# Performance work log

Measured on AMD Instinct MI355X. Metric: run time of the kernel, lower is better.

The kernel has to match this reference:

```python
import jax, jax.numpy as jnp
import numpy as np

# config
BSZ, L_, DM = 4, 2048, 1024
H, G, P, N, R = 16, 4, 64, 64, 2
RATIO = H // G            # 4
E, K = 64, 2              # kmoe experts / top_k
DPROJ = H * P * 2 + G * N * R * 2 + G * 3  # 3084


def rms(x, w, eps=1e-5):
    return x * jax.lax.rsqrt(jnp.mean(x * x, axis=-1, keepdims=True) + eps) * w


def kron_moe(x, router_w, A_e, B_e, scale, bias, d1, d2, o1, o2, k):
    # x: [..., d1*d2] -> [..., o1*o2]
    orig = x.shape
    xf = x.reshape(-1, d1 * d2)
    logits = xf @ router_w.T                       # [T, E]
    vals, idx = jax.lax.top_k(logits, k)           # [T, k]
    probs = jax.nn.softmax(vals, axis=-1)
    xs = xf.reshape(-1, d1, d2)
    # Y[t,k,o,p] = sum_ij A[t,k,o,i] x[t,i,j] B[t,k,p,j]
    Y = jnp.einsum('tkoi,tij,tkpj->tkop', A_e[idx], xs, B_e[idx])
    out = jnp.sum(Y * probs[:, :, None, None], axis=1).reshape(orig[:-1] + (o1 * o2,))
    return out * scale + bias


def setup_inputs() -> dict:
    key = jax.random.key(0)
    ks = jax.random.split(key, 12)
    r = lambda k, s, sc: jax.random.normal(k, s, jnp.float32) * sc
    return dict(
        u=jax.random.normal(ks[0], (BSZ, L_, DM), jnp.float32),
        in_proj_w=r(ks[1], (DPROJ, DM), 0.02),
        in_proj_b=jnp.zeros((DPROJ,), jnp.float32),
        xup_router=r(ks[2], (E, P), 0.02),
        xup_A=r(ks[3], (E, 8, 8), 0.1),
        xup_B=r(ks[4], (E, 16, 8), 0.1),
        xup_scale=jnp.ones((1,), jnp.float32),
        xup_bias=jnp.zeros((P * R,), jnp.float32),
        ydown_w=r(ks[5], (P, P * R), 0.02),
        oup_router=r(ks[6], (E, H * P), 0.02),
        oup_A=r(ks[7], (E, 32, 32), 0.05),
        oup_B=r(ks[8], (E, 32, 32), 0.05),
        oup_scale=jnp.ones((1,), jnp.float32),
        oup_bias=jnp.zeros((DM,), jnp.float32),
        theta_log=r(ks[9], (G, N // 2), 1.0),
        D=jnp.ones((H,), jnp.float32),
        normB_w=jnp.ones((N * R,), jnp.float32),
        normC_w=jnp.ones((N * R,), jnp.float32),
        bias_B=jnp.zeros((G, N, R), jnp.float32),
        bias_C=jnp.zeros((G, N, R), jnp.float32),
        pregate_w=jnp.ones((H * P,), jnp.float32),
    )


def reference(u, in_proj_w, in_proj_b, xup_router, xup_A, xup_B, xup_scale, xup_bias,
              ydown_w, oup_router, oup_A, oup_B, oup_scale, oup_bias,
              theta_log, D, normB_w, normC_w, bias_B, bias_C, pregate_w):
    B, L, _ = u.shape
    HP, GNR = H * P, G * N * R
    proj = u @ in_proj_w.T + in_proj_b
    splits = np.cumsum([HP, HP, GNR, GNR, G, G])
    z, x_p, Bp, Cp, dt, A_p, lam = jnp.split(proj, splits, axis=-1)
    dt = jax.nn.softplus(dt)                       # [B,L,G]
    A = -jnp.exp(A_p)                              # [B,L,G]
    theta = jnp.exp(theta_log)                     # [G,N/2]
    Bp = rms(Bp.reshape(B, L, G, N * R), normB_w).reshape(B, L, G, N, R) + bias_B
    Cp = rms(Cp.reshape(B, L, G, N * R), normC_w).reshape(B, L, G, N, R) + bias_C
    angles_g = jnp.cumsum(dt[..., None] * theta[None, None], axis=1)   # [B,L,G,N/2]
    rep = lambda v: jnp.repeat(v, RATIO, axis=2)   # group -> head broadcast
    angles = rep(angles_g)                         # [B,L,H,N/2]
    dt_h = rep(dt[..., None])                      # [B,L,H,1]
    A_h = rep(A[..., None])                        # [B,L,H,1]
    B_h, C_h = rep(Bp), rep(Cp)                    # [B,L,H,N,R]
    cos = jnp.cos(angles)[..., None]
    sin = jnp.sin(angles)[..., None]

    def rotate(v):
        re, im = v[..., 0::2, :], v[..., 1::2, :]
        return jnp.stack([re * cos - im * sin, re * sin + im * cos], axis=-2).reshape(v.shape)

    B_rot, C_rot = rotate(B_h), rotate(C_h)
    x = kron_moe(x_p.reshape(B, L, H, P), xup_router, xup_A, xup_B, xup_scale, xup_bias,
                 8, 8, 8, 16, K).reshape(B, L, H, P, R)
    alpha = jnp.exp(dt_h * A_h)[..., None]         # [B,L,H,1,1]

    mv = lambda v: jnp.moveaxis(v, 1, 0)           # time-major for scan

    def step(h, xs):
        Br, Cr, xt, at, dtt = xs
        in_sig = jnp.einsum('bhnr,bhpr->bhnp', Br, xt)
        h = h * at + dtt[..., None] * in_sig
        y_t = jnp.einsum('bhnp,bhnr->bhpr', h, Cr)
        return h, y_t

    h0 = jnp.zeros((B, H, N, P), u.dtype)
    _, ys = jax.lax.scan(step, h0, (mv(B_rot), mv(C_rot), mv(x), mv(alpha), mv(dt_h)))
    y = jnp.moveaxis(ys, 0, 1)                     # [B,L,H,P,R]
    y = (y.reshape(B, L, H, P * R) @ ydown_w.T).reshape(B, L, H * P)
    y = rms(y + x_p * jnp.repeat(D, P), pregate_w) * jax.nn.sigmoid(z)
    out = kron_moe(y, oup_router, oup_A, oup_B, oup_scale, oup_bias, 32, 32, 32, 32, K)
    return out
```

## Files before the change

kernel.cpp:

```cpp
#include <hip/hip_runtime.h>
#include <hip/hip_bf16.h>
#include <math.h>

namespace {
constexpr int kB = 4, kL = 2048, kDM = 1024;
constexpr int kH = 16, kG = 4;
constexpr int kDPROJ = 3084;
constexpr int COL_Z = 0, COL_XP = 1024, COL_B = 2048, COL_C = 2560, COL_DT = 3072, COL_A = 3076;
constexpr int kTOK = kB * kL;
constexpr int kNC = kL / 64;
constexpr int kNPAD = 3200;
constexpr float kLOG2E = 1.4426950408889634f;
}

typedef __attribute__((ext_vector_type(8))) __bf16 bf16x8;
typedef __attribute__((ext_vector_type(8))) unsigned short u16x8;
typedef __attribute__((ext_vector_type(4))) float f32x4;

#define GLDS16(gp, lp)                                                          \
  __builtin_amdgcn_global_load_lds(                                             \
      (const __attribute__((address_space(1))) void*)(gp),                      \
      (__attribute__((address_space(3))) void*)(lp), 16, 0, 0)

__device__ __forceinline__ unsigned short bf16_rne(float f) {
  unsigned u = __builtin_bit_cast(unsigned, f);
  unsigned r = u + 0x7fffu + ((u >> 16) & 1u);
  return (unsigned short)(r >> 16);
}
__device__ __forceinline__ void split2(float f, unsigned short& h, unsigned short& l) {
  unsigned short hh = bf16_rne(f);
  float hf = __builtin_bit_cast(float, (unsigned)hh << 16);
  h = hh;
  l = bf16_rne(f - hf);
}
__device__ __forceinline__ bf16x8 ldsb8(const unsigned short* p) {
  return __builtin_bit_cast(bf16x8, *(const u16x8*)p);
}

__global__ __launch_bounds__(256) void k_split_u(const float* __restrict__ X,
                                                 unsigned short* __restrict__ hi,
                                                 unsigned short* __restrict__ lo) {
  int i = blockIdx.x * 256 + threadIdx.x;
  float4 x = ((const float4*)X)[i];
  float xs[4] = {x.x, x.y, x.z, x.w};
  ushort4 hv, lv;
  unsigned short hq[4], lq[4];
#pragma unroll
  for (int q = 0; q < 4; ++q) split2(xs[q], hq[q], lq[q]);
  hv.x = hq[0]; hv.y = hq[1]; hv.z = hq[2]; hv.w = hq[3];
  lv.x = lq[0]; lv.y = lq[1]; lv.z = lq[2]; lv.w = lq[3];
  ((ushort4*)hi)[i] = hv;
  ((ushort4*)lo)[i] = lv;
}

__global__ __launch_bounds__(256) void k_split_w(const float* __restrict__ X,
                                                 unsigned short* __restrict__ hi,
                                                 unsigned short* __restrict__ lo) {
  int i = blockIdx.x * 256 + threadIdx.x;
  int row = i >> 8;
  float4 x = make_float4(0.f, 0.f, 0.f, 0.f);
  if (row < kDPROJ) x = ((const float4*)X)[i];
  float xs[4] = {x.x, x.y, x.z, x.w};
  ushort4 hv, lv;
  unsigned short hq[4], lq[4];
#pragma unroll
  for (int q = 0; q < 4; ++q) split2(xs[q], hq[q], lq[q]);
  hv.x = hq[0]; hv.y = hq[1]; hv.z = hq[2]; hv.w = hq[3];
  lv.x = lq[0]; lv.y = lq[1]; lv.z = lq[2]; lv.w = lq[3];
  ((ushort4*)hi)[i] = hv;
  ((ushort4*)lo)[i] = lv;
}

__global__ __launch_bounds__(256) void k_inproj_mfma(
    const unsigned short* __restrict__ Uhi, const unsigned short* __restrict__ Ulo,
    const unsigned short* __restrict__ Whi, const unsigned short* __restrict__ Wlo,
    const float* __restrict__ bias, float* __restrict__ proj,
    float* __restrict__ dtA) {
  __shared__ unsigned short lds_u[16384];
  const int tid = threadIdx.x;
  const int wave = tid >> 6, lane = tid & 63;
  const int wm = wave >> 1, wn = wave & 1;
  const int row0 = blockIdx.x * 128, col0 = blockIdx.y * 128;
  const int fr = lane & 15, kq = lane >> 4;

  f32x4 acc[4][4];
#pragma unroll
  for (int i = 0; i < 4; ++i)
#pragma unroll
    for (int j = 0; j < 4; ++j) acc[i][j] = (f32x4){0.f, 0.f, 0.f, 0.f};

  const int s0 = wave * 64 + lane;

  for (int k0 = 0; k0 < kDM; k0 += 32) {
#pragma unroll
    for (int q = 0; q < 2; ++q) {
      const int slot = q * 256 + s0;
      const int r = slot >> 2;
      const int ce = ((slot & 3) ^ ((r >> 1) & 3)) * 8;
      const size_t ao = (size_t)(row0 + r) * kDM + k0 + ce;
      const size_t bo = (size_t)(col0 + r) * kDM + k0 + ce;
      const int lb = (q * 256 + wave * 64) * 16;
      GLDS16(Uhi + ao, (char*)lds_u + lb);
      GLDS16(Ulo + ao, (char*)lds_u + 8192 + lb);
      GLDS16(Whi + bo, (char*)lds_u + 16384 + lb);
      GLDS16(Wlo + bo, (char*)lds_u + 24576 + lb);
    }
    __syncthreads();
    bf16x8 ahi[4], alo[4], bhi[4], blo[4];
#pragma unroll
    for (int mi = 0; mi < 4; ++mi) {
      int r = wm * 64 + mi * 16 + fr;
      int off = r * 32 + ((kq ^ ((r >> 1) & 3)) * 8);
      ahi[mi] = ldsb8(lds_u + off);
      alo[mi] = ldsb8(lds_u + 4096 + off);
    }
#pragma unroll
    for (int ni = 0; ni < 4; ++ni) {
      int r = wn * 64 + ni * 16 + fr;
      int off = r * 32 + ((kq ^ ((r >> 1) & 3)) * 8);
      bhi[ni] = ldsb8(lds_u + 8192 + off);
      blo[ni] = ldsb8(lds_u + 12288 + off);
    }
#pragma unroll
    for (int mi = 0; mi < 4; ++mi)
#pragma unroll
      for (int ni = 0; ni < 4; ++ni) {
        acc[mi][ni] = __builtin_amdgcn_mfma_f32_16x16x32_bf16(ahi[mi], bhi[ni], acc[mi][ni], 0, 0, 0);
        acc[mi][ni] = __builtin_amdgcn_mfma_f32_16x16x32_bf16(ahi[mi], blo[ni], acc[mi][ni], 0, 0, 0);
        acc[mi][ni] = __builtin_amdgcn_mfma_f32_16x16x32_bf16(alo[mi], bhi[ni], acc[mi][ni], 0, 0, 0);
      }
    __syncthreads();
  }

  const int orow = row0 + wm * 64, ocol = col0 + wn * 64;
#pragma unroll
  for (int mi = 0; mi < 4; ++mi)
#pragma unroll
    for (int ni = 0; ni < 4; ++ni) {
      int cg = ocol + ni * 16 + fr;
      if (cg < kDPROJ) {
        float bv = bias[cg];
#pragma unroll
        for (int r = 0; r < 4; ++r) {
          int rg = orow + mi * 16 + kq * 4 + r;
          float v = acc[mi][ni][r] + bv;
          proj[(size_t)rg * kDPROJ + cg] = v;
          if (cg >= COL_DT && cg < COL_DT + 8)
            dtA[(size_t)rg * 8 + (cg - COL_DT)] = v;
        }
      }
    }
}

__global__ __launch_bounds__(256) void k_dtprep(const float* __restrict__ dtA,
                                                float* __restrict__ dtg,
                                                float* __restrict__ cumalog,
                                                double* __restrict__ cumdt) {
  int bg = blockIdx.x;
  int b = bg / kG, g = bg % kG;
  int tid = threadIdx.x;
  __shared__ double s_dt[256], s_al[256];
  double loc_dt[8], loc_al[8];
  double sdt = 0.0, sal = 0.0;
#pragma unroll
  for (int q = 0; q < 8; ++q) {
    int t = tid * 8 + q;
    size_t i = (size_t)(b * kL + t) * 8;
    float rd = dtA[i + g];
    float ra = dtA[i + 4 + g];
    float dt = rd > 20.f ? rd : log1pf(expf(rd));
    float al = -expf(ra) * dt;
    dtg[(size_t)(b * kL + t) * kG + g] = dt;
    sdt += (double)dt; loc_dt[q] = sdt;
    sal += (double)al; loc_al[q] = sal;
  }
  s_dt[tid] = sdt; s_al[tid] = sal;
  __syncthreads();
  for (int off = 1; off < 256; off <<= 1) {
    double a = 0.0, c = 0.0;
    if (tid >= off) { a = s_dt[tid - off]; c = s_al[tid - off]; }
    __syncthreads();
    s_dt[tid] += a; s_al[tid] += c;
    __syncthreads();
  }
  double base_dt = tid ? s_dt[tid - 1] : 0.0;
  double base_al = tid ? s_al[tid - 1] : 0.0;
#pragma unroll
  for (int q = 0; q < 8; ++q) {
    int t = tid * 8 + q;
    size_t idx = (size_t)(b * kL + t) * kG + g;
    cumdt[idx] = base_dt + loc_dt[q];
    cumalog[idx] = (float)(base_al + loc_al[q]);
  }
}

__global__ __launch_bounds__(256) void k_angles(const double* __restrict__ cumdt,
                                                const float* __restrict__ theta_log,
                                                float* __restrict__ cs_tab) {
  int idx = blockIdx.x * 256 + threadIdx.x;
  int tok = idx >> 7, gk = idx & 127, g = gk >> 5, k = gk & 31;
  double theta = exp((double)theta_log[g * 32 + k]);
  double ang = theta * cumdt[(size_t)tok * kG + g];
  const double twopi = 6.283185307179586476925286766559;
  double rem = ang - floor(ang / twopi) * twopi;
  cs_tab[(size_t)idx * 2] = cosf((float)rem);
  cs_tab[(size_t)idx * 2 + 1] = sinf((float)rem);
}

__global__ __launch_bounds__(1024) void k_rotate(float* __restrict__ proj,
                                                 const float* __restrict__ cs_tab,
                                                 const float* __restrict__ normB_w,
                                                 const float* __restrict__ normC_w,
                                                 const float* __restrict__ bias_B,
                                                 const float* __restrict__ bias_C) {
  int tok = blockIdx.x;
  int tid = threadIdx.x;
  __shared__ float buf[1024];
  __shared__ float red[16];
  size_t rowoff = (size_t)tok * kDPROJ;
  int g = tid >> 8;
  int half = (tid >> 7) & 1;
  int j = tid & 127;
  int wave = tid >> 6;
  int col = (half ? COL_C : COL_B) + g * 128 + j;
  float v = proj[rowoff + col];
  float ss = v * v;
  for (int o = 1; o < 64; o <<= 1) ss += __shfl_xor(ss, o);
  if ((tid & 63) == 0) red[wave] = ss;
  __syncthreads();
  float tot = red[wave] + red[wave ^ 1];
  float scale = rsqrtf(tot / 128.f + 1e-5f);
  const float* nw = half ? normC_w : normB_w;
  const float* bb = half ? bias_C : bias_B;
  float nv = v * scale * nw[j] + bb[g * 128 + j];
  buf[tid] = nv;
  __syncthreads();
  float other = buf[tid ^ 2];
  int n = j >> 1;
  int k = n >> 1;
  bool isRe = (n & 1) == 0;
  const float* cs = cs_tab + (((size_t)tok * kG + g) * 32 + k) * 2;
  float cc = cs[0], sn = cs[1];
  float out = isRe ? (nv * cc - other * sn) : (other * sn + nv * cc);
  proj[rowoff + col] = out;
}

__global__ __launch_bounds__(256) void k_xup(const float* __restrict__ proj,
                                             const float* __restrict__ router,
                                             const float* __restrict__ Ae,
                                             const float* __restrict__ Be,
                                             const float* __restrict__ scale_,
                                             const float* __restrict__ bias_,
                                             float* __restrict__ xmoe) {
  int wave = threadIdx.x >> 6, lane = threadIdx.x & 63;
  int unit = blockIdx.x * 4 + wave;
  int tok = unit >> 4, h = unit & 15;
  __shared__ double Rd[64][65];
  __shared__ double xs_d[4][64];
  __shared__ float  xs_f[4][65];
  for (int m = threadIdx.x; m < 4096; m += 256)
    Rd[m >> 6][m & 63] = (double)router[m];
  float xv = proj[(size_t)tok * kDPROJ + COL_XP + h * 64 + lane];
  xs_d[wave][lane] = (double)xv;
  xs_f[wave][lane] = xv;
  __syncthreads();
  double a0 = 0.0, a1 = 0.0, a2 = 0.0, a3 = 0.0;
#pragma unroll
  for (int d = 0; d < 64; d += 4) {
    a0 += Rd[lane][d + 0] * xs_d[wave][d + 0];
    a1 += Rd[lane][d + 1] * xs_d[wave][d + 1];
    a2 += Rd[lane][d + 2] * xs_d[wave][d + 2];
    a3 += Rd[lane][d + 3] * xs_d[wave][d + 3];
  }
  float logit = (float)((a0 + a1) + (a2 + a3));
  float v1 = logit; int i1 = lane;
  for (int o = 1; o < 64; o <<= 1) {
    float vv = __shfl_xor(v1, o); int ii = __shfl_xor(i1, o);
    if (vv > v1 || (vv == v1 && ii < i1)) { v1 = vv; i1 = ii; }
  }
  float lm = (lane == i1) ? -INFINITY : logit;
  float v2 = lm; int i2 = lane;
  for (int o = 1; o < 64; o <<= 1) {
    float vv = __shfl_xor(v2, o); int ii = __shfl_xor(i2, o);
    if (vv > v2 || (vv == v2 && ii < i2)) { v2 = vv; i2 = ii; }
  }
  int e1 = __builtin_amdgcn_readfirstlane(i1);
  int e2 = __builtin_amdgcn_readfirstlane(i2);
  float e12 = expf(v2 - v1);
  float p1 = 1.f / (1.f + e12), p2 = e12 / (1.f + e12);
  const int p = lane & 15, o = lane >> 4;
  float out0 = 0.f, out1 = 0.f;
#pragma unroll
  for (int kk = 0; kk < 2; ++kk) {
    int e = kk ? e2 : e1;
    float pw = kk ? p2 : p1;
    const float4* Bp = (const float4*)(Be + (size_t)e * 128 + p * 8);
    float4 b0 = Bp[0], b1 = Bp[1];
    const float4* Ar = (const float4*)(Ae + (size_t)e * 64);
    float4 A0a = Ar[o * 2], A0b = Ar[o * 2 + 1];
    float4 A1a = Ar[(o + 4) * 2], A1b = Ar[(o + 4) * 2 + 1];
    float Ar0[8] = {A0a.x, A0a.y, A0a.z, A0a.w, A0b.x, A0b.y, A0b.z, A0b.w};
    float Ar1[8] = {A1a.x, A1a.y, A1a.z, A1a.w, A1b.x, A1b.y, A1b.z, A1b.w};
    float y0 = 0.f, y1 = 0.f;
#pragma unroll
    for (int i = 0; i < 8; ++i) {
      const float* xp = &xs_f[wave][i * 8];
      float t = xp[0] * b0.x + xp[1] * b0.y + xp[2] * b0.z + xp[3] * b0.w
              + xp[4] * b1.x + xp[5] * b1.y + xp[6] * b1.z + xp[7] * b1.w;
      y0 += Ar0[i] * t;
      y1 += Ar1[i] * t;
    }
    out0 += pw * y0;
    out1 += pw * y1;
  }
  float sc = scale_[0];
  size_t ob = (size_t)unit * 128;
  xmoe[ob + lane] = out0 * sc + bias_[lane];
  xmoe[ob + lane + 64] = out1 * sc + bias_[lane + 64];
}

namespace { constexpr int SK = 136; }
__global__ __launch_bounds__(256) void k_passA(const float* __restrict__ proj,
                                               const float* __restrict__ xmoe,
                                               const float* __restrict__ dtg,
                                               const float* __restrict__ cumalog,
                                               float* __restrict__ hstate) {
  __shared__ unsigned short sBh[64 * SK];
  __shared__ unsigned short sBl[64 * SK];
  __shared__ unsigned short sXh[64 * SK];
  __shared__ unsigned short sXl[64 * SK];
  __shared__ float wv[64];
  int bid = blockIdx.x;
  int c = bid & 31, h = (bid >> 5) & 15, b = bid >> 9, g = h >> 2;
  int tid = threadIdx.x;
  const int wave = tid >> 6, lane = tid & 63;
  const int fr = lane & 15, kq = lane >> 4;
  int base = c * 64;
  size_t tok0 = (size_t)b * kL + base;
  if (tid < 64) {
    float ca_last = cumalog[(tok0 + 63) * kG + g];
    float ca_s = cumalog[(tok0 + tid) * kG + g];
    float dt = dtg[(tok0 + tid) * kG + g];
    wv[tid] = expf(ca_last - ca_s) * dt;
  }
  __syncthreads();
  for (int m = tid; m < 8192; m += 256) {
    int s = m >> 7, j = m & 127;
    int k = s * 2 + (j & 1), n = j >> 1;
    unsigned short hh, ll;
    float bval = proj[(tok0 + s) * kDPROJ + COL_B + g * 128 + j] * wv[s];
    split2(bval, hh, ll);
    sBh[n * SK + k] = hh; sBl[n * SK + k] = ll;
    float xval = xmoe[((tok0 + s) * kH + h) * (size_t)128 + j];
    split2(xval, hh, ll);
    sXh[n * SK + k] = hh; sXl[n * SK + k] = ll;
  }
  __syncthreads();
  const int n0 = wave * 16;
  f32x4 acc[4];
#pragma unroll
  for (int j = 0; j < 4; ++j) acc[j] = (f32x4){0.f, 0.f, 0.f, 0.f};
#pragma unroll
  for (int ks = 0; ks < 4; ++ks) {
    int kb = ks * 32 + kq * 8;
    int offA = (n0 + fr) * SK + kb;
    bf16x8 ah = ldsb8(sBh + offA);
    bf16x8 al = ldsb8(sBl + offA);
#pragma unroll
    for (int ni = 0; ni < 4; ++ni) {
      int offB = (ni * 16 + fr) * SK + kb;
      bf16x8 bh = ldsb8(sXh + offB);
      bf16x8 bl = ldsb8(sXl + offB);
      acc[ni] = __builtin_amdgcn_mfma_f32_16x16x32_bf16(ah, bh, acc[ni], 0, 0, 0);
      acc[ni] = __builtin_amdgcn_mfma_f32_16x16x32_bf16(ah, bl, acc[ni], 0, 0, 0);
      acc[ni] = __builtin_amdgcn_mfma_f32_16x16x32_bf16(al, bh, acc[ni], 0, 0, 0);
    }
  }
  float* out = hstate + (size_t)bid * 4096;
#pragma unroll
  for (int ni = 0; ni < 4; ++ni)
#pragma unroll
    for (int r = 0; r < 4; ++r) {
      int n = n0 + kq * 4 + r;
      int p = ni * 16 + fr;
      out[n * 64 + p] = acc[ni][r];
    }
}

__global__ __launch_bounds__(256) void k_passB(float* __restrict__ hstate,
                                               const float* __restrict__ cumalog) {
  int bid = blockIdx.x;
  int q8 = bid & 7, bh = bid >> 3;
  int b = bh >> 4, g = (bh & 15) >> 2;
  int tid = threadIdx.x;
  float hrun[2] = {0.f, 0.f};
  float* Hbase = hstate + (size_t)bh * 32 * 4096 + q8 * 512;
  for (int c = 0; c < 32; ++c) {
    float ca_last = cumalog[((size_t)b * kL + c * 64 + 63) * kG + g];
    float ca_prev = c ? cumalog[((size_t)b * kL + c * 64 - 1) * kG + g] : 0.f;
    float Dc = expf(ca_last - ca_prev);
    float* Hc = Hbase + (size_t)c * 4096;
#pragma unroll
    for (int q = 0; q < 2; ++q) {
      int idx = tid + q * 256;
      float local = Hc[idx];
      Hc[idx] = hrun[q];
      hrun[q] = Dc * hrun[q] + local;
    }
  }
}

namespace {
constexpr int SC = 72;
constexpr int SG = 136;
constexpr int SH = 72;
constexpr int SW = 66;
}
__global__ __launch_bounds__(1024) void k_passC(const float* __restrict__ proj,
                                                const float* __restrict__ xmoe,
                                                const float* __restrict__ dtg,
                                                const float* __restrict__ cumalog,
                                                const float* __restrict__ hstate,
                                                const float* __restrict__ ydown,
                                                float* __restrict__ outY) {
  __shared__ __align__(16) char smem[162560];
  unsigned short* sCh = (unsigned short*)smem;
  unsigned short* sCl = sCh + 128 * SC;
  unsigned short* sBh = (unsigned short*)(smem + 36864);
  unsigned short* sBl = sBh + 128 * SC;
  float*          sW  = (float*)(smem + 73728);
  unsigned short* sHh = (unsigned short*)(smem + 73728);
  unsigned short* sHl = sHh + 64 * SH;
  unsigned short* sGh = (unsigned short*)(smem + 92160);
  unsigned short* sGl = sGh + 128 * SG;
  float* sca  = (float*)(smem + 161792);
  float* sdts = sca + 64;
  float* selx = sdts + 64;
  unsigned short* sXh  = (unsigned short*)smem;
  unsigned short* sXl  = sXh + 64 * SG;
  unsigned short* sWdh = (unsigned short*)(smem + 36864);
  unsigned short* sWdl = sWdh + 64 * SG;
  unsigned short* sYh  = (unsigned short*)(smem + 92160);
  unsigned short* sYl  = sYh + 64 * SG;

  int bid = blockIdx.x;
  int c = bid & 31, h = (bid >> 5) & 15, b = bid >> 9, g = h >> 2;
  int tid = threadIdx.x;
  const int wave = tid >> 6, lane = tid & 63;
  const int fr = lane & 15, kq = lane >> 4;
  int base = c * 64;
  size_t tok0 = (size_t)b * kL + base;
  size_t projBase = tok0 * kDPROJ;

  if (tid < 64) {
    float ca_prev = base ? cumalog[(tok0 - 1) * kG + g] : 0.f;
    float ca_t = cumalog[(tok0 + tid) * kG + g];
    sca[tid] = ca_t;
    sdts[tid] = dtg[(tok0 + tid) * kG + g];
    selx[tid] = exp2f((ca_t - ca_prev) * kLOG2E);
  }
  for (int m = tid; m < 8192; m += 1024) {
    int s = m >> 7, j = m & 127;
    int row = s * 2 + (j & 1), col = j >> 1;
    unsigned short hh, ll;
    float cv = proj[projBase + (size_t)s * kDPROJ + COL_C + g * 128 + j];
    split2(cv, hh, ll);
    sCh[row * SC + col] = hh; sCl[row * SC + col] = ll;
    float bv = proj[projBase + (size_t)s * kDPROJ + COL_B + g * 128 + j];
    split2(bv, hh, ll);
    sBh[row * SC + col] = hh; sBl[row * SC + col] = ll;
  }
  __syncthreads();

  for (int m = tid; m < 4096; m += 1024) {
    int t = m >> 6, s = m & 63;
    float w = (s <= t) ? sdts[s] * exp2f((sca[t] - sca[s]) * kLOG2E) : 0.f;
    sW[t * SW + s] = w;
  }
  const int rowA0 = (wave & 7) * 16;
  const int colH = wave >> 3;
  f32x4 gacc[4];
#pragma unroll
  for (int j = 0; j < 4; ++j) gacc[j] = (f32x4){0.f, 0.f, 0.f, 0.f};
#pragma unroll
  for (int ks = 0; ks < 2; ++ks) {
    int kb = ks * 32 + kq * 8;
    int offA = (rowA0 + fr) * SC + kb;
    bf16x8 ah = ldsb8(sCh + offA);
    bf16x8 al = ldsb8(sCl + offA);
#pragma unroll
    for (int ni = 0; ni < 4; ++ni) {
      int off = (colH * 64 + ni * 16 + fr) * SC + kb;
      bf16x8 bh = ldsb8(sBh + off);
      bf16x8 bl = ldsb8(sBl + off);
      gacc[ni] = __builtin_amdgcn_mfma_f32_16x16x32_bf16(ah, bh, gacc[ni], 0, 0, 0);
      gacc[ni] = __builtin_amdgcn_mfma_f32_16x16x32_bf16(ah, bl, gacc[ni], 0, 0, 0);
      gacc[ni] = __builtin_amdgcn_mfma_f32_16x16x32_bf16(al, bh, gacc[ni], 0, 0, 0);
    }
  }
  __syncthreads();

#pragma unroll
  for (int ni = 0; ni < 4; ++ni) {
    int colg = colH * 64 + ni * 16 + fr;
    int s = colg >> 1;
#pragma unroll
    for (int r = 0; r < 4; ++r) {
      int rowg = rowA0 + kq * 4 + r;
      int t = rowg >> 1;
      float gm = gacc[ni][r] * sW[t * SW + s];
      unsigned short hh, ll;
      split2(gm, hh, ll);
      sGh[rowg * SG + colg] = hh;
      sGl[rowg * SG + colg] = ll;
    }
  }
  __syncthreads();

  for (int m = tid; m < 4096; m += 1024) {
    int n = m >> 6, p = m & 63;
    float v = hstate[(size_t)bid * 4096 + m];
    unsigned short hh, ll;
    split2(v, hh, ll);
    sHh[p * SH + n] = hh;
    sHl[p * SH + n] = ll;
  }
  __syncthreads();

  f32x4 yac[2];
#pragma unroll
  for (int j = 0; j < 2; ++j) yac[j] = (f32x4){0.f, 0.f, 0.f, 0.f};
#pragma unroll
  for (int ks = 0; ks < 2; ++ks) {
    int kb = ks * 32 + kq * 8;
    int offA = (rowA0 + fr) * SC + kb;
    bf16x8 ah = ldsb8(sCh + offA);
    bf16x8 al = ldsb8(sCl + offA);
#pragma unroll
    for (int ni = 0; ni < 2; ++ni) {
      int off = (colH * 32 + ni * 16 + fr) * SH + kb;
      bf16x8 bh = ldsb8(sHh + off);
      bf16x8 bl = ldsb8(sHl + off);
      yac[ni] = __builtin_amdgcn_mfma_f32_16x16x32_bf16(ah, bh, yac[ni], 0, 0, 0);
      yac[ni] = __builtin_amdgcn_mfma_f32_16x16x32_bf16(ah, bl, yac[ni], 0, 0, 0);
      yac[ni] = __builtin_amdgcn_mfma_f32_16x16x32_bf16(al, bh, yac[ni], 0, 0, 0);
    }
  }
#pragma unroll
  for (int r = 0; r < 4; ++r) {
    int t = (rowA0 + kq * 4 + r) >> 1;
    float e = selx[t];
#pragma unroll
    for (int ni = 0; ni < 2; ++ni) yac[ni][r] *= e;
  }
  __syncthreads();

  for (int m = tid; m < 8192; m += 1024) {
    int s = m >> 7, j = m & 127;
    float xv = xmoe[((tok0 + s) * kH + h) * (size_t)128 + j];
    int p = j >> 1, cc = s * 2 + (j & 1);
    unsigned short hh, ll;
    split2(xv, hh, ll);
    sXh[p * SG + cc] = hh; sXl[p * SG + cc] = ll;
    float wv2 = ydown[m];
    split2(wv2, hh, ll);
    sWdh[(m >> 7) * SG + (m & 127)] = hh;
    sWdl[(m >> 7) * SG + (m & 127)] = ll;
  }
  __syncthreads();

#pragma unroll
  for (int ks = 0; ks < 4; ++ks) {
    int kb = ks * 32 + kq * 8;
    int offA = (rowA0 + fr) * SG + kb;
    bf16x8 ah = ldsb8(sGh + offA);
    bf16x8 al = ldsb8(sGl + offA);
#pragma unroll
    for (int ni = 0; ni < 2; ++ni) {
      int off = (colH * 32 + ni * 16 + fr) * SG + kb;
      bf16x8 bh = ldsb8(sXh + off);
      bf16x8 bl = ldsb8(sXl + off);
      yac[ni] = __builtin_amdgcn_mfma_f32_16x16x32_bf16(ah, bh, yac[ni], 0, 0, 0);
      yac[ni] = __builtin_amdgcn_mfma_f32_16x16x32_bf16(ah, bl, yac[ni], 0, 0, 0);
      yac[ni] = __builtin_amdgcn_mfma_f32_16x16x32_bf16(al, bh, yac[ni], 0, 0, 0);
    }
  }
  __syncthreads();

#pragma unroll
  for (int ni = 0; ni < 2; ++ni)
#pragma unroll
    for (int r = 0; r < 4; ++r) {
      int rowg = rowA0 + kq * 4 + r;
      int t = rowg >> 1, rr = rowg & 1;
      int p = colH * 32 + ni * 16 + fr;
      unsigned short hh, ll;
      split2(yac[ni][r], hh, ll);
      sYh[t * SG + p * 2 + rr] = hh;
      sYl[t * SG + p * 2 + rr] = ll;
    }
  __syncthreads();

  f32x4 zac = (f32x4){0.f, 0.f, 0.f, 0.f};
  const int zr0 = (wave & 3) * 16, zc0 = (wave >> 2) * 16;
#pragma unroll
  for (int ks = 0; ks < 4; ++ks) {
    int kb = ks * 32 + kq * 8;
    int offA = (zr0 + fr) * SG + kb;
    bf16x8 ah = ldsb8(sYh + offA);
    bf16x8 al = ldsb8(sYl + offA);
    int offB = (zc0 + fr) * SG + kb;
    bf16x8 bh = ldsb8(sWdh + offB);
    bf16x8 bl = ldsb8(sWdl + offB);
    zac = __builtin_amdgcn_mfma_f32_16x16x32_bf16(ah, bh, zac, 0, 0, 0);
    zac = __builtin_amdgcn_mfma_f32_16x16x32_bf16(ah, bl, zac, 0, 0, 0);
    zac = __builtin_amdgcn_mfma_f32_16x16x32_bf16(al, bh, zac, 0, 0, 0);
  }
#pragma unroll
  for (int r = 0; r < 4; ++r) {
    int t = zr0 + kq * 4 + r;
    int o = zc0 + fr;
    outY[(tok0 + t) * (size_t)1024 + h * 64 + o] = zac[r];
  }
}

__global__ __launch_bounds__(256) void k_gate(float* __restrict__ y,
                                              const float* __restrict__ proj,
                                              const float* __restrict__ Dv,
                                              const float* __restrict__ pregate_w) {
  int tok = blockIdx.x;
  int tid = threadIdx.x;
  size_t yoff = (size_t)tok * 1024;
  size_t poff = (size_t)tok * kDPROJ;
  __shared__ float red[4];
  float vals[4];
  float ss = 0.f;
#pragma unroll
  for (int q = 0; q < 4; ++q) {
    int j = tid + q * 256;
    float v = y[yoff + j] + proj[poff + COL_XP + j] * Dv[j >> 6];
    vals[q] = v;
    ss += v * v;
  }
  for (int o = 1; o < 64; o <<= 1) ss += __shfl_xor(ss, o);
  if ((tid & 63) == 0) red[tid >> 6] = ss;
  __syncthreads();
  float tot = red[0] + red[1] + red[2] + red[3];
  float scale = rsqrtf(tot / 1024.f + 1e-5f);
#pragma unroll
  for (int q = 0; q < 4; ++q) {
    int j = tid + q * 256;
    float z = proj[poff + COL_Z + j];
    float sig = 1.f / (1.f + expf(-z));
    y[yoff + j] = vals[q] * scale * pregate_w[j] * sig;
  }
}

__global__ __launch_bounds__(256) void k_logits(const float* __restrict__ y,
                                                const float* __restrict__ router,
                                                float* __restrict__ logits) {
  __shared__ float Yt[16][65];
  __shared__ float Rt[64][65];
  int tid = threadIdx.x;
  int tok0 = blockIdx.x * 16;
  int t = tid & 15;
  int e0 = (tid >> 4) * 4;
  double acc[4] = {0.0, 0.0, 0.0, 0.0};
  for (int kc = 0; kc < 1024; kc += 64) {
    for (int m = tid; m < 1024; m += 256) {
      int tt = m >> 6, c = m & 63;
      Yt[tt][c] = y[(size_t)(tok0 + tt) * 1024 + kc + c];
    }
    for (int m = tid; m < 4096; m += 256) {
      int ee = m >> 6, c = m & 63;
      Rt[ee][c] = router[(size_t)ee * 1024 + kc + c];
    }
    __syncthreads();
    for (int c = 0; c < 64; ++c) {
      float yv = Yt[t][c];
#pragma unroll
      for (int i = 0; i < 4; ++i)
        acc[i] += (double)Rt[e0 + i][c] * (double)yv;
    }
    __syncthreads();
  }
#pragma unroll
  for (int i = 0; i < 4; ++i)
    logits[(size_t)(tok0 + t) * 64 + e0 + i] = (float)acc[i];
}

__global__ __launch_bounds__(256) void k_oup(float* __restrict__ y,
                                             const float* __restrict__ logits,
                                             const float* __restrict__ Ae,
                                             const float* __restrict__ Be,
                                             const float* __restrict__ scale_,
                                             const float* __restrict__ bias_) {
  int tok = blockIdx.x;
  int tid = threadIdx.x;
  __shared__ float xs[1024];
  __shared__ float Ts[32][33];
  __shared__ float lg[64];
  size_t yoff = (size_t)tok * 1024;
  for (int m = tid; m < 1024; m += 256) xs[m] = y[yoff + m];
  if (tid < 64) lg[tid] = logits[(size_t)tok * 64 + tid];
  __syncthreads();
  float v1 = -INFINITY; int i1 = -1;
  for (int e = 0; e < 64; ++e) { float v = lg[e]; if (v > v1) { v1 = v; i1 = e; } }
  float v2 = -INFINITY; int i2 = -1;
  for (int e = 0; e < 64; ++e) { if (e == i1) continue; float v = lg[e]; if (v > v2) { v2 = v; i2 = e; } }
  float e12 = expf(v2 - v1);
  float p1 = 1.f / (1.f + e12), p2 = e12 / (1.f + e12);
  float out[4] = {0.f, 0.f, 0.f, 0.f};
  for (int kk = 0; kk < 2; ++kk) {
    int e = kk ? i2 : i1;
    float pw = kk ? p2 : p1;
    const float* A = Ae + (size_t)e * 1024;
    const float* Bm = Be + (size_t)e * 1024;
    __syncthreads();
    for (int m = tid; m < 1024; m += 256) {
      int i = m >> 5, p = m & 31;
      float t = 0.f;
#pragma unroll
      for (int j = 0; j < 32; ++j) t += xs[i * 32 + j] * Bm[p * 32 + j];
      Ts[i][p] = t;
    }
    __syncthreads();
#pragma unroll
    for (int q = 0; q < 4; ++q) {
      int cc = tid + q * 256;
      int o = cc >> 5, p = cc & 31;
      float a2 = 0.f;
#pragma unroll
      for (int i = 0; i < 32; ++i) a2 += A[o * 32 + i] * Ts[i][p];
      out[q] += pw * a2;
    }
  }
  float sc = scale_[0];
#pragma unroll
  for (int q = 0; q < 4; ++q) {
    int cc = tid + q * 256;
    y[yoff + cc] = out[q] * sc + bias_[cc];
  }
}

extern "C" void kernel_launch(void* const* d_in, const int* in_sizes, int n_in,
                              void* d_out, int out_size, void* d_ws, size_t ws_size,
                              hipStream_t stream) {
  const float* u          = (const float*)d_in[0];
  const float* in_proj_w  = (const float*)d_in[1];
  const float* in_proj_b  = (const float*)d_in[2];
  const float* xup_router = (const float*)d_in[3];
  const float* xup_A      = (const float*)d_in[4];
  const float* xup_B      = (const float*)d_in[5];
  const float* xup_scale  = (const float*)d_in[6];
  const float* xup_bias   = (const float*)d_in[7];
  const float* ydown_w    = (const float*)d_in[8];
  const float* oup_router = (const float*)d_in[9];
  const float* oup_A      = (const float*)d_in[10];
  const float* oup_B      = (const float*)d_in[11];
  const float* oup_scale  = (const float*)d_in[12];
  const float* oup_bias   = (const float*)d_in[13];
  const float* theta_log  = (const float*)d_in[14];
  const float* Dv         = (const float*)d_in[15];
  const float* normB_w    = (const float*)d_in[16];
  const float* normC_w    = (const float*)d_in[17];
  const float* bias_B     = (const float*)d_in[18];
  const float* bias_C     = (const float*)d_in[19];
  const float* pregate_w  = (const float*)d_in[20];

  char* ws = (char*)d_ws;
  float* proj = (float*)ws;      ws += (size_t)kTOK * kDPROJ * 4;
  float* dtg = (float*)ws;       ws += (size_t)kTOK * kG * 4;
  float* cumalog = (float*)ws;   ws += (size_t)kTOK * kG * 4;
  double* cumdt = (double*)ws;   ws += (size_t)kTOK * kG * 8;
  float* dtA = (float*)ws;       ws += (size_t)kTOK * 8 * 4;
  float* cs_tab = (float*)ws;    ws += (size_t)kTOK * kG * 32 * 2 * 4;
  float* xmoe = (float*)ws;      ws += (size_t)kTOK * kH * 128 * 4;
  float* hstate = (float*)ws;    ws += (size_t)kB * kH * kNC * 4096 * 4;
  float* outY = (float*)d_out;

  float* logits = cs_tab;

  unsigned short* Uhi = (unsigned short*)xmoe;
  unsigned short* Ulo = Uhi + (size_t)kTOK * kDM;
  unsigned short* Whi = Ulo + (size_t)kTOK * kDM;
  unsigned short* Wlo = Whi + (size_t)kNPAD * kDM;

  k_split_u<<<dim3(kTOK * kDM / 4 / 256), dim3(256), 0, stream>>>(u, Uhi, Ulo);
  k_split_w<<<dim3(kNPAD * kDM / 4 / 256), dim3(256), 0, stream>>>(in_proj_w, Whi, Wlo);
  k_inproj_mfma<<<dim3(kTOK / 128, kNPAD / 128), dim3(256), 0, stream>>>(Uhi, Ulo, Whi, Wlo, in_proj_b, proj, dtA);
  k_dtprep<<<dim3(kB * kG), dim3(256), 0, stream>>>(dtA, dtg, cumalog, cumdt);
  k_angles<<<dim3(kTOK * 128 / 256), dim3(256), 0, stream>>>(cumdt, theta_log, cs_tab);
  k_rotate<<<dim3(kTOK), dim3(1024), 0, stream>>>(proj, cs_tab, normB_w, normC_w, bias_B, bias_C);
  k_xup<<<dim3(kTOK * kH / 4), dim3(256), 0, stream>>>(proj, xup_router, xup_A, xup_B, xup_scale, xup_bias, xmoe);
  k_passA<<<dim3(kB * kH * kNC), dim3(256), 0, stream>>>(proj, xmoe, dtg, cumalog, hstate);
  k_passB<<<dim3(kB * kH * 8), dim3(256), 0, stream>>>(hstate, cumalog);
  k_passC<<<dim3(kB * kH * kNC), dim3(1024), 0, stream>>>(proj, xmoe, dtg, cumalog, hstate, ydown_w, outY);
  k_gate<<<dim3(kTOK), dim3(256), 0, stream>>>(outY, proj, Dv, pregate_w);
  k_logits<<<dim3(kTOK / 16), dim3(256), 0, stream>>>(outY, oup_router, logits);
  k_oup<<<dim3(kTOK), dim3(256), 0, stream>>>(outY, logits, oup_A, oup_B, oup_scale, oup_bias);
}
```

Measured before the change: 913.9 us.

## Split xup router logits into a separate per-token kernel with shared router tile

The xup MoE kernel loaded the full 64x64 router into shared memory as doubles for every 4-head block. It now has two kernels. One computes router logits per token, covering all 16 heads, from a float router tile shared by 16 heads, and writes them to a scratch buffer that reuses hstate. The second kernel reads those logits and does top-k and the Kronecker apply. This cuts redundant router loads and double-precision shared-memory traffic, at the cost of an extra launch and a logits round trip through global memory.

Result: faster. 876.3 us (-4.1%).

```diff
diff --git a/kernel.cpp b/kernel.cpp
--- a/kernel.cpp
+++ b/kernel.cpp
@@ -245,34 +245,51 @@
   proj[rowoff + col] = out;
 }
 
-__global__ __launch_bounds__(256) void k_xup(const float* __restrict__ proj,
-                                             const float* __restrict__ router,
-                                             const float* __restrict__ Ae,
-                                             const float* __restrict__ Be,
-                                             const float* __restrict__ scale_,
-                                             const float* __restrict__ bias_,
-                                             float* __restrict__ xmoe) {
+__global__ __launch_bounds__(256) void k_xlogits(const float* __restrict__ proj,
+                                                 const float* __restrict__ router,
+                                                 float* __restrict__ logits) {
+  __shared__ float Yt[16][65];
+  __shared__ float Rt[64][65];
+  int tid = threadIdx.x;
+  int tok = blockIdx.x;
+  for (int m = tid; m < 1024; m += 256)
+    Yt[m >> 6][m & 63] = proj[(size_t)tok * kDPROJ + COL_XP + m];
+  for (int m = tid; m < 4096; m += 256)
+    Rt[m >> 6][m & 63] = router[m];
+  __syncthreads();
+  int t = tid & 15;
+  int e0 = (tid >> 4) * 4;
+  float lg[4];
+#pragma unroll
+  for (int e = 0; e < 4; ++e) {
+    double a0 = 0.0, a1 = 0.0, a2 = 0.0, a3 = 0.0;
+#pragma unroll
+    for (int d = 0; d < 64; d += 4) {
+      a0 += (double)Rt[e0 + e][d + 0] * (double)Yt[t][d + 0];
+      a1 += (double)Rt[e0 + e][d + 1] * (double)Yt[t][d + 1];
+      a2 += (double)Rt[e0 + e][d + 2] * (double)Yt[t][d + 2];
+      a3 += (double)Rt[e0 + e][d + 3] * (double)Yt[t][d + 3];
+    }
+    lg[e] = (float)((a0 + a1) + (a2 + a3));
+  }
+  float4 out = make_float4(lg[0], lg[1], lg[2], lg[3]);
+  *(float4*)&logits[((size_t)tok * 16 + t) * 64 + e0] = out;
+}
+
+__global__ __launch_bounds__(256) void k_xapply(const float* __restrict__ proj,
+                                                const float* __restrict__ logits,
+                                                const float* __restrict__ Ae,
+                                                const float* __restrict__ Be,
+                                                const float* __restrict__ scale_,
+                                                const float* __restrict__ bias_,
+                                                float* __restrict__ xmoe) {
   int wave = threadIdx.x >> 6, lane = threadIdx.x & 63;
   int unit = blockIdx.x * 4 + wave;
   int tok = unit >> 4, h = unit & 15;
-  __shared__ double Rd[64][65];
-  __shared__ double xs_d[4][64];
-  __shared__ float  xs_f[4][65];
-  for (int m = threadIdx.x; m < 4096; m += 256)
-    Rd[m >> 6][m & 63] = (double)router[m];
+  __shared__ float xs_f[4][65];
   float xv = proj[(size_t)tok * kDPROJ + COL_XP + h * 64 + lane];
-  xs_d[wave][lane] = (double)xv;
   xs_f[wave][lane] = xv;
-  __syncthreads();
-  double a0 = 0.0, a1 = 0.0, a2 = 0.0, a3 = 0.0;
-#pragma unroll
-  for (int d = 0; d < 64; d += 4) {
-    a0 += Rd[lane][d + 0] * xs_d[wave][d + 0];
-    a1 += Rd[lane][d + 1] * xs_d[wave][d + 1];
-    a2 += Rd[lane][d + 2] * xs_d[wave][d + 2];
-    a3 += Rd[lane][d + 3] * xs_d[wave][d + 3];
-  }
-  float logit = (float)((a0 + a1) + (a2 + a3));
+  float logit = logits[(size_t)unit * 64 + lane];
   float v1 = logit; int i1 = lane;
   for (int o = 1; o < 64; o <<= 1) {
     float vv = __shfl_xor(v1, o); int ii = __shfl_xor(i1, o);
@@ -780,6 +797,7 @@
   float* outY = (float*)d_out;
 
   float* logits = cs_tab;
+  float* logits_x = hstate;
 
   unsigned short* Uhi = (unsigned short*)xmoe;
   unsigned short* Ulo = Uhi + (size_t)kTOK * kDM;
@@ -792,7 +810,8 @@
   k_dtprep<<<dim3(kB * kG), dim3(256), 0, stream>>>(dtA, dtg, cumalog, cumdt);
   k_angles<<<dim3(kTOK * 128 / 256), dim3(256), 0, stream>>>(cumdt, theta_log, cs_tab);
   k_rotate<<<dim3(kTOK), dim3(1024), 0, stream>>>(proj, cs_tab, normB_w, normC_w, bias_B, bias_C);
-  k_xup<<<dim3(kTOK * kH / 4), dim3(256), 0, stream>>>(proj, xup_router, xup_A, xup_B, xup_scale, xup_bias, xmoe);
+  k_xlogits<<<dim3(kTOK), dim3(256), 0, stream>>>(proj, xup_router, logits_x);
+  k_xapply<<<dim3(kTOK * kH / 4), dim3(256), 0, stream>>>(proj, logits_x, xup_A, xup_B, xup_scale, xup_bias, xmoe);
   k_passA<<<dim3(kB * kH * kNC), dim3(256), 0, stream>>>(proj, xmoe, dtg, cumalog, hstate);
   k_passB<<<dim3(kB * kH * 8), dim3(256), 0, stream>>>(hstate, cumalog);
   k_passC<<<dim3(kB * kH * kNC), dim3(1024), 0, stream>>>(proj, xmoe, dtg, cumalog, hstate, ydown_w, outY);
```
